# Performance work log

Hardware: AMD Instinct MI355X
Metric: run time of the kernel (lower is better)

## Reference

```python
import jax, jax.numpy as jnp
import numpy as np

N, E, D = 100000, 1600000, 256  # nodes, edges, feature dim
BN_EPS = 1e-5


def _bn(x, g, b):
    # training-mode batchnorm over the node axis (biased variance)
    m = jnp.mean(x, axis=0)
    v = jnp.var(x, axis=0)
    return (x - m) * jax.lax.rsqrt(v + BN_EPS) * g + b


def _gin_layer(h, src, dst, w1, b1, g1, be1, w2, b2, g2=None, be2=None):
    # (1 + eps) * h + sum over in-neighbors; eps = 0
    agg = h + jax.ops.segment_sum(h[src], dst, num_segments=N)
    # MLP(2): Linear -> BN -> ReLU -> Linear
    z = jax.nn.relu(_bn(agg @ w1 + b1, g1, be1))
    z = z @ w2 + b2
    # ApplyNodeFunc wrapper (all but last layer): BN -> ReLU
    if g2 is not None:
        z = jax.nn.relu(_bn(z, g2, be2))
    return z


def setup_inputs() -> dict:
    key = jax.random.key(0)
    ks = jax.random.split(key, 16)
    inp = {}
    inp["x"] = jax.random.normal(ks[0], (N, D), jnp.float32)
    inp["src"] = jax.random.randint(ks[1], (E,), 0, N)
    inp["dst"] = jax.random.randint(ks[2], (E,), 0, N)
    i = 3
    for l in range(3):
        inp[f"l{l}_w1"] = jax.random.normal(ks[i], (D, D), jnp.float32) * 0.02; i += 1
        inp[f"l{l}_b1"] = jnp.zeros((D,), jnp.float32)
        inp[f"l{l}_g1"] = jnp.ones((D,), jnp.float32)
        inp[f"l{l}_be1"] = jnp.zeros((D,), jnp.float32)
        inp[f"l{l}_w2"] = jax.random.normal(ks[i], (D, D), jnp.float32) * 0.02; i += 1
        inp[f"l{l}_b2"] = jnp.zeros((D,), jnp.float32)
        if l < 2:  # last layer: bare MLP, no outer BN/ReLU
            inp[f"l{l}_g2"] = jnp.ones((D,), jnp.float32)
            inp[f"l{l}_be2"] = jnp.zeros((D,), jnp.float32)
    return inp


def reference(x, src, dst,
              l0_w1, l0_b1, l0_g1, l0_be1, l0_w2, l0_b2, l0_g2, l0_be2,
              l1_w1, l1_b1, l1_g1, l1_be1, l1_w2, l1_b2, l1_g2, l1_be2,
              l2_w1, l2_b1, l2_g1, l2_be1, l2_w2, l2_b2):
    # dropout p=0.0 -> identity; residual=False
    h = _gin_layer(x, src, dst, l0_w1, l0_b1, l0_g1, l0_be1, l0_w2, l0_b2, l0_g2, l0_be2)
    h = _gin_layer(h, src, dst, l1_w1, l1_b1, l1_g1, l1_be1, l1_w2, l1_b2, l1_g2, l1_be2)
    h = _gin_layer(h, src, dst, l2_w1, l2_b1, l2_g1, l2_be1, l2_w2, l2_b2)
    return h
```

## Files before the change

kernel.cpp:

```cpp
#include <hip/hip_runtime.h>
#include <hip/hip_bf16.h>
#include <stdint.h>

#define NN 100000
#define DD 256
#define EE 1600000
#define NB 391

typedef short s16x8 __attribute__((ext_vector_type(8)));
typedef float f32x4 __attribute__((ext_vector_type(4)));

__device__ __forceinline__ unsigned short f2bf(float f) {
    union { float f; unsigned int u; } un; un.f = f;
    unsigned int u = un.u;
    unsigned int r = u + 0x7fffu + ((u >> 16) & 1u);
    return (unsigned short)(r >> 16);
}
__device__ __forceinline__ float bf2f(unsigned short s) {
    union { unsigned int u; float f; } c; c.u = (unsigned int)s << 16; return c.f;
}

__global__ void k_wconv(const float* __restrict__ W, unsigned short* __restrict__ Wf) {
    int t = blockIdx.x * 256 + threadIdx.x;
    int j = t & 7;
    int l = (t >> 3) & 63;
    int c = (t >> 9) & 15;
    int s = t >> 13;
    int k   = s * 32 + (l >> 4) * 8 + j;
    int col = c * 16 + (l & 15);
    Wf[t] = f2bf(W[k * 256 + col]);
}

__global__ void k_deghist(const int* __restrict__ dst, int* __restrict__ deg) {
    int e = blockIdx.x * 256 + threadIdx.x;
    atomicAdd(&deg[dst[e]], 1);
}

__global__ void k_blocksum(const int* __restrict__ deg, int* __restrict__ bsum) {
    __shared__ int s[256];
    int t = blockIdx.x * 256 + threadIdx.x;
    s[threadIdx.x] = (t < NN) ? deg[t] : 0;
    __syncthreads();
    for (int off = 128; off > 0; off >>= 1) {
        if (threadIdx.x < off) s[threadIdx.x] += s[threadIdx.x + off];
        __syncthreads();
    }
    if (threadIdx.x == 0) bsum[blockIdx.x] = s[0];
}

__global__ void k_scanb(const int* __restrict__ bsum, int* __restrict__ boff,
                        int* __restrict__ rowptr) {
    __shared__ int s[512];
    int tid = threadIdx.x;
    s[tid] = (tid < NB) ? bsum[tid] : 0;
    __syncthreads();
    for (int off = 1; off < 512; off <<= 1) {
        int x = 0;
        if (tid >= off) x = s[tid - off];
        __syncthreads();
        if (tid >= off) s[tid] += x;
        __syncthreads();
    }
    if (tid < NB) boff[tid] = (tid > 0) ? s[tid - 1] : 0;
    if (tid == 0) rowptr[NN] = EE;
}

__global__ void k_finalscan(const int* __restrict__ deg, const int* __restrict__ boff,
                            int* __restrict__ rowptr) {
    __shared__ int s[256];
    int tid = threadIdx.x;
    int t = blockIdx.x * 256 + tid;
    int v = (t < NN) ? deg[t] : 0;
    s[tid] = v;
    __syncthreads();
    for (int off = 1; off < 256; off <<= 1) {
        int x = 0;
        if (tid >= off) x = s[tid - off];
        __syncthreads();
        if (tid >= off) s[tid] += x;
        __syncthreads();
    }
    if (t < NN) rowptr[t] = boff[blockIdx.x] + s[tid] - v;
}

__global__ void k_fill(const int* __restrict__ src, const int* __restrict__ dst,
                       const int* __restrict__ rowptr, int* __restrict__ cur,
                       int* __restrict__ eidx) {
    int e = blockIdx.x * 256 + threadIdx.x;
    int d = dst[e];
    int pos = atomicAdd(&cur[d], 1);
    eidx[rowptr[d] + pos] = src[e];
}

template<int MODE>
__launch_bounds__(256)
__global__ void k_gather(const void* __restrict__ hv, const int* __restrict__ rowptr,
                         const int* __restrict__ eidx,
                         const float* __restrict__ s1, const float* __restrict__ s2,
                         const float* __restrict__ g, const float* __restrict__ be,
                         ushort4* __restrict__ agg) {
    int gid = blockIdx.x * 256 + threadIdx.x;
    int node = gid >> 6;
    int lane = gid & 63;
    if (node >= NN) return;
    int beg = rowptr[node];
    int end = rowptr[node + 1];
    float4 acc;

    if constexpr (MODE == 0) {
        const float4* h = (const float4*)hv;
        acc = h[(size_t)node * 64 + lane];
        int i = beg;
        for (; i + 8 <= end; i += 8) {
            int idx[8];
            #pragma unroll
            for (int j = 0; j < 8; j++) idx[j] = eidx[i + j];
            float4 v[8];
            #pragma unroll
            for (int j = 0; j < 8; j++) v[j] = h[(size_t)idx[j] * 64 + lane];
            #pragma unroll
            for (int j = 0; j < 8; j++) {
                acc.x += v[j].x; acc.y += v[j].y; acc.z += v[j].z; acc.w += v[j].w;
            }
        }
        for (; i + 4 <= end; i += 4) {
            int idx[4];
            #pragma unroll
            for (int j = 0; j < 4; j++) idx[j] = eidx[i + j];
            float4 v[4];
            #pragma unroll
            for (int j = 0; j < 4; j++) v[j] = h[(size_t)idx[j] * 64 + lane];
            #pragma unroll
            for (int j = 0; j < 4; j++) {
                acc.x += v[j].x; acc.y += v[j].y; acc.z += v[j].z; acc.w += v[j].w;
            }
        }
        for (; i + 2 <= end; i += 2) {
            float4 v0 = h[(size_t)eidx[i] * 64 + lane];
            float4 v1 = h[(size_t)eidx[i + 1] * 64 + lane];
            acc.x += v0.x + v1.x; acc.y += v0.y + v1.y;
            acc.z += v0.z + v1.z; acc.w += v0.w + v1.w;
        }
        if (i < end) {
            float4 v = h[(size_t)eidx[i] * 64 + lane];
            acc.x += v.x; acc.y += v.y; acc.z += v.z; acc.w += v.w;
        }
    } else {
        const ushort4* h = (const ushort4*)hv;
        int c0 = lane * 4;
        float4 s1v = *(const float4*)(s1 + c0);
        float4 s2v = *(const float4*)(s2 + c0);
        float4 gv  = *(const float4*)(g + c0);
        float4 bev = *(const float4*)(be + c0);
        float kk[4], sh[4];
        {
            float m, var;
            m = s1v.x * (1.f/NN); var = s2v.x * (1.f/NN) - m*m; kk[0] = rsqrtf(var+1e-5f)*gv.x; sh[0] = bev.x - m*kk[0];
            m = s1v.y * (1.f/NN); var = s2v.y * (1.f/NN) - m*m; kk[1] = rsqrtf(var+1e-5f)*gv.y; sh[1] = bev.y - m*kk[1];
            m = s1v.z * (1.f/NN); var = s2v.z * (1.f/NN) - m*m; kk[2] = rsqrtf(var+1e-5f)*gv.z; sh[2] = bev.z - m*kk[2];
            m = s1v.w * (1.f/NN); var = s2v.w * (1.f/NN) - m*m; kk[3] = rsqrtf(var+1e-5f)*gv.w; sh[3] = bev.w - m*kk[3];
        }
        ushort4 u = h[(size_t)node * 64 + lane];
        acc.x = fmaxf(bf2f(u.x) * kk[0] + sh[0], 0.f);
        acc.y = fmaxf(bf2f(u.y) * kk[1] + sh[1], 0.f);
        acc.z = fmaxf(bf2f(u.z) * kk[2] + sh[2], 0.f);
        acc.w = fmaxf(bf2f(u.w) * kk[3] + sh[3], 0.f);
        int i = beg;
        for (; i + 8 <= end; i += 8) {
            int idx[8];
            #pragma unroll
            for (int j = 0; j < 8; j++) idx[j] = eidx[i + j];
            ushort4 v[8];
            #pragma unroll
            for (int j = 0; j < 8; j++) v[j] = h[(size_t)idx[j] * 64 + lane];
            #pragma unroll
            for (int j = 0; j < 8; j++) {
                acc.x += fmaxf(bf2f(v[j].x) * kk[0] + sh[0], 0.f);
                acc.y += fmaxf(bf2f(v[j].y) * kk[1] + sh[1], 0.f);
                acc.z += fmaxf(bf2f(v[j].z) * kk[2] + sh[2], 0.f);
                acc.w += fmaxf(bf2f(v[j].w) * kk[3] + sh[3], 0.f);
            }
        }
        for (; i + 4 <= end; i += 4) {
            int idx[4];
            #pragma unroll
            for (int j = 0; j < 4; j++) idx[j] = eidx[i + j];
            ushort4 v[4];
            #pragma unroll
            for (int j = 0; j < 4; j++) v[j] = h[(size_t)idx[j] * 64 + lane];
            #pragma unroll
            for (int j = 0; j < 4; j++) {
                acc.x += fmaxf(bf2f(v[j].x) * kk[0] + sh[0], 0.f);
                acc.y += fmaxf(bf2f(v[j].y) * kk[1] + sh[1], 0.f);
                acc.z += fmaxf(bf2f(v[j].z) * kk[2] + sh[2], 0.f);
                acc.w += fmaxf(bf2f(v[j].w) * kk[3] + sh[3], 0.f);
            }
        }
        for (; i < end; i++) {
            ushort4 a = h[(size_t)eidx[i] * 64 + lane];
            acc.x += fmaxf(bf2f(a.x) * kk[0] + sh[0], 0.f);
            acc.y += fmaxf(bf2f(a.y) * kk[1] + sh[1], 0.f);
            acc.z += fmaxf(bf2f(a.z) * kk[2] + sh[2], 0.f);
            acc.w += fmaxf(bf2f(a.w) * kk[3] + sh[3], 0.f);
        }
    }
    ushort4 o;
    o.x = f2bf(acc.x); o.y = f2bf(acc.y); o.z = f2bf(acc.z); o.w = f2bf(acc.w);
    agg[(size_t)node * 64 + lane] = o;
}

template<bool ABF16, bool BNSTAGE, bool OUTBF16, bool STATS>
__launch_bounds__(256)
__global__ void k_gemm(const void* __restrict__ Av, const unsigned short* __restrict__ Wf,
                       const float* __restrict__ bias,
                       const float* __restrict__ s1, const float* __restrict__ s2,
                       const float* __restrict__ g, const float* __restrict__ be,
                       void* __restrict__ Cv,
                       float* __restrict__ s1o, float* __restrict__ s2o, int M) {
    __shared__ s16x8 Al[2048];
    __shared__ float sbn[512];
    const int tid = threadIdx.x;
    const int base_row = blockIdx.x * 64;

    if constexpr (STATS) {
        sbn[tid] = 0.f; sbn[tid + 256] = 0.f;
    }

    #pragma unroll
    for (int i = 0; i < 8; i++) {
        int chunk = tid + i * 256;
        int row = chunk >> 5;
        int k0  = (chunk & 31) * 8;
        int gr = base_row + row;
        s16x8 sv;
        if constexpr (ABF16) {
            if (gr < M)
                sv = *(const s16x8*)((const unsigned short*)Av + (size_t)gr * 256 + k0);
            else
                sv = (s16x8){0,0,0,0,0,0,0,0};
        } else {
            float vv[8];
            if (gr < M) {
                const float4* gp = (const float4*)((const float*)Av + (size_t)gr * 256 + k0);
                float4 v0 = gp[0], v1 = gp[1];
                vv[0]=v0.x; vv[1]=v0.y; vv[2]=v0.z; vv[3]=v0.w;
                vv[4]=v1.x; vv[5]=v1.y; vv[6]=v1.z; vv[7]=v1.w;
            } else {
                #pragma unroll
                for (int j = 0; j < 8; j++) vv[j] = 0.f;
            }
            if constexpr (BNSTAGE) {
                #pragma unroll
                for (int j = 0; j < 8; j++) {
                    float m  = s1[k0+j] * (1.f/NN);
                    float var = s2[k0+j] * (1.f/NN) - m*m;
                    float kk = rsqrtf(var + 1e-5f) * g[k0+j];
                    float shv = be[k0+j] - m * kk;
                    vv[j] = fmaxf(vv[j] * kk + shv, 0.f);
                }
            }
            #pragma unroll
            for (int j = 0; j < 8; j++) sv[j] = (short)f2bf(vv[j]);
        }
        int byte = (row * 512 + k0 * 2) ^ ((row & 7) << 4);
        Al[byte >> 4] = sv;
    }
    __syncthreads();

    const int lane = tid & 63;
    const int w = tid >> 6;
    const int wr = w >> 1;
    const int wc = w & 1;

    f32x4 acc[2][8];
    #pragma unroll
    for (int m = 0; m < 2; m++)
        #pragma unroll
        for (int c = 0; c < 8; c++)
            acc[m][c] = (f32x4){0.f, 0.f, 0.f, 0.f};

    #pragma unroll
    for (int s = 0; s < 8; s++) {
        s16x8 a[2], b[8];
        #pragma unroll
        for (int m = 0; m < 2; m++) {
            int row = wr * 32 + m * 16 + (lane & 15);
            int koff = s * 32 + (lane >> 4) * 8;
            int byte = (row * 512 + koff * 2) ^ ((row & 7) << 4);
            a[m] = Al[byte >> 4];
        }
        const unsigned short* wp = Wf + (size_t)((s * 16 + wc * 8) * 64 + lane) * 8;
        #pragma unroll
        for (int c = 0; c < 8; c++)
            b[c] = *(const s16x8*)(wp + (size_t)c * 512);
        #pragma unroll
        for (int m = 0; m < 2; m++)
            #pragma unroll
            for (int c = 0; c < 8; c++)
                acc[m][c] = __builtin_amdgcn_mfma_f32_16x16x32_bf16(a[m], b[c], acc[m][c], 0, 0, 0);
    }

    #pragma unroll
    for (int m = 0; m < 2; m++) {
        int row0 = base_row + wr * 32 + m * 16 + (lane >> 4) * 4;
        #pragma unroll
        for (int c = 0; c < 8; c++) {
            int col = wc * 128 + c * 16 + (lane & 15);
            float bv = bias[col];
            float p1 = 0.f, p2 = 0.f;
            #pragma unroll
            for (int r = 0; r < 4; r++) {
                int row = row0 + r;
                if (row < M) {
                    float v = acc[m][c][r] + bv;
                    if constexpr (OUTBF16)
                        ((unsigned short*)Cv)[(size_t)row * 256 + col] = f2bf(v);
                    else
                        ((float*)Cv)[(size_t)row * 256 + col] = v;
                    if constexpr (STATS) { p1 += v; p2 += v * v; }
                }
            }
            if constexpr (STATS) {
                p1 += __shfl_xor(p1, 16); p1 += __shfl_xor(p1, 32);
                p2 += __shfl_xor(p2, 16); p2 += __shfl_xor(p2, 32);
                if (lane < 16) {
                    atomicAdd(&sbn[col], p1);
                    atomicAdd(&sbn[col + 256], p2);
                }
            }
        }
    }
    if constexpr (STATS) {
        __syncthreads();
        atomicAdd(&s1o[tid & 255], sbn[tid]);
        atomicAdd(&s2o[tid & 255], sbn[tid + 256]);
    }
}

extern "C" void kernel_launch(void* const* d_in, const int* in_sizes, int n_in,
                              void* d_out, int out_size, void* d_ws, size_t ws_size,
                              hipStream_t stream) {
    const float* x   = (const float*)d_in[0];
    const int*   src = (const int*)d_in[1];
    const int*   dst = (const int*)d_in[2];
    const float* W[6]    = { (const float*)d_in[3],  (const float*)d_in[7],
                             (const float*)d_in[11], (const float*)d_in[15],
                             (const float*)d_in[19], (const float*)d_in[23] };
    const float* Bias[6] = { (const float*)d_in[4],  (const float*)d_in[8],
                             (const float*)d_in[12], (const float*)d_in[16],
                             (const float*)d_in[20], (const float*)d_in[24] };
    const float* Gam[5]  = { (const float*)d_in[5],  (const float*)d_in[9],
                             (const float*)d_in[13], (const float*)d_in[17],
                             (const float*)d_in[21] };
    const float* Bet[5]  = { (const float*)d_in[6],  (const float*)d_in[10],
                             (const float*)d_in[14], (const float*)d_in[18],
                             (const float*)d_in[22] };

    char* ws = (char*)d_ws;
    unsigned short* Wf = (unsigned short*)ws;
    float* stats = (float*)(ws + 786432);
    unsigned short* aggbf = (unsigned short*)(ws + (1 << 20));
    unsigned short* z2bf  = aggbf + (size_t)NN * DD;
    char* csr = ws + (1 << 20) + 102400000;
    int* rowptr = (int*)csr;
    int* deg    = (int*)(csr + 400128);
    int* cur    = (int*)(csr + 800128);
    int* bsum   = (int*)(csr + 1200128);
    int* boff   = (int*)(csr + 1202176);
    int* eidx   = (int*)(csr + 1204224);
    float* OUT = (float*)d_out;

    for (int i = 0; i < 6; i++)
        k_wconv<<<256, 256, 0, stream>>>(W[i], Wf + (size_t)i * 65536);
    hipMemsetAsync(stats, 0, 5 * 512 * sizeof(float), stream);
    hipMemsetAsync(deg, 0, NN * sizeof(int), stream);
    hipMemsetAsync(cur, 0, NN * sizeof(int), stream);

    k_deghist<<<EE / 256, 256, 0, stream>>>(dst, deg);
    k_blocksum<<<NB, 256, 0, stream>>>(deg, bsum);
    k_scanb<<<1, 512, 0, stream>>>(bsum, boff, rowptr);
    k_finalscan<<<NB, 256, 0, stream>>>(deg, boff, rowptr);
    k_fill<<<EE / 256, 256, 0, stream>>>(src, dst, rowptr, cur, eidx);

    const int GG = (NN * 64 + 255) / 256;
    float* st[5];
    for (int i = 0; i < 5; i++) st[i] = stats + i * 512;

    auto gemm1 = [&](const unsigned short* A, int wi, int si, float* C) {
        k_gemm<true, false, false, true><<<1563, 256, 0, stream>>>(
            A, Wf + (size_t)wi * 65536, Bias[wi], nullptr, nullptr, nullptr, nullptr,
            C, st[si], st[si] + 256, NN);
    };
    auto gemm2bf = [&](const float* A, int wi, int si, int so, unsigned short* C) {
        k_gemm<false, true, true, true><<<1563, 256, 0, stream>>>(
            A, Wf + (size_t)wi * 65536, Bias[wi], st[si], st[si] + 256, Gam[si], Bet[si],
            C, st[so], st[so] + 256, NN);
    };

    k_gather<0><<<GG, 256, 0, stream>>>(x, rowptr, eidx, nullptr, nullptr, nullptr, nullptr,
                                        (ushort4*)aggbf);
    gemm1(aggbf, 0, 0, OUT);
    gemm2bf(OUT, 1, 0, 1, z2bf);

    k_gather<1><<<GG, 256, 0, stream>>>(z2bf, rowptr, eidx, st[1], st[1] + 256, Gam[1], Bet[1],
                                        (ushort4*)aggbf);
    gemm1(aggbf, 2, 2, OUT);
    gemm2bf(OUT, 3, 2, 3, z2bf);

    k_gather<1><<<GG, 256, 0, stream>>>(z2bf, rowptr, eidx, st[3], st[3] + 256, Gam[3], Bet[3],
                                        (ushort4*)aggbf);
    gemm1(aggbf, 4, 4, OUT);
    k_gemm<false, true, false, false><<<1563, 256, 0, stream>>>(
        OUT, Wf + (size_t)5 * 65536, Bias[5], st[4], st[4] + 256, Gam[4], Bet[4],
        OUT, nullptr, nullptr, NN);
}
```

Before: 1.150 ms.

## Feature-slice the gather kernel and convert input features to bf16 first

Gather is restructured so each block handles one of 8 column slices (32 features) for 64 nodes. Within a wave, 4 groups of 16 lanes split the edge list and combine partial sums with shuffles, so each gathered row piece is a 64-byte read. The input x is first converted to bf16 so layer 0 gathers half the bytes. Slicing by features is meant to keep the per-slice working set small enough to hit in L2, and parallelising over edges cuts the serial chain per node. In exchange it adds a conversion pass, extra bf16 rounding of layer-0 inputs, and shorter, less coalesced memory transactions.

```diff
diff --git a/kernel.cpp b/kernel.cpp
--- a/kernel.cpp
+++ b/kernel.cpp
@@ -29,6 +29,15 @@
     int k   = s * 32 + (l >> 4) * 8 + j;
     int col = c * 16 + (l & 15);
     Wf[t] = f2bf(W[k * 256 + col]);
+}
+
+__global__ void k_tobf16(const float4* __restrict__ in, ushort4* __restrict__ out, int n) {
+    for (int i = blockIdx.x * 256 + threadIdx.x; i < n; i += gridDim.x * 256) {
+        float4 v = in[i];
+        ushort4 o;
+        o.x = f2bf(v.x); o.y = f2bf(v.y); o.z = f2bf(v.z); o.w = f2bf(v.w);
+        out[i] = o;
+    }
 }
 
 __global__ void k_deghist(const int* __restrict__ dst, int* __restrict__ deg) {
@@ -94,119 +103,87 @@
 
 template<int MODE>
 __launch_bounds__(256)
-__global__ void k_gather(const void* __restrict__ hv, const int* __restrict__ rowptr,
+__global__ void k_gather(const ushort2* __restrict__ h, const int* __restrict__ rowptr,
                          const int* __restrict__ eidx,
                          const float* __restrict__ s1, const float* __restrict__ s2,
                          const float* __restrict__ g, const float* __restrict__ be,
-                         ushort4* __restrict__ agg) {
-    int gid = blockIdx.x * 256 + threadIdx.x;
-    int node = gid >> 6;
-    int lane = gid & 63;
-    if (node >= NN) return;
-    int beg = rowptr[node];
-    int end = rowptr[node + 1];
-    float4 acc;
-
-    if constexpr (MODE == 0) {
-        const float4* h = (const float4*)hv;
-        acc = h[(size_t)node * 64 + lane];
-        int i = beg;
-        for (; i + 8 <= end; i += 8) {
-            int idx[8];
-            #pragma unroll
-            for (int j = 0; j < 8; j++) idx[j] = eidx[i + j];
-            float4 v[8];
-            #pragma unroll
-            for (int j = 0; j < 8; j++) v[j] = h[(size_t)idx[j] * 64 + lane];
-            #pragma unroll
-            for (int j = 0; j < 8; j++) {
-                acc.x += v[j].x; acc.y += v[j].y; acc.z += v[j].z; acc.w += v[j].w;
-            }
-        }
-        for (; i + 4 <= end; i += 4) {
-            int idx[4];
-            #pragma unroll
-            for (int j = 0; j < 4; j++) idx[j] = eidx[i + j];
-            float4 v[4];
-            #pragma unroll
-            for (int j = 0; j < 4; j++) v[j] = h[(size_t)idx[j] * 64 + lane];
-            #pragma unroll
-            for (int j = 0; j < 4; j++) {
-                acc.x += v[j].x; acc.y += v[j].y; acc.z += v[j].z; acc.w += v[j].w;
-            }
-        }
-        for (; i + 2 <= end; i += 2) {
-            float4 v0 = h[(size_t)eidx[i] * 64 + lane];
-            float4 v1 = h[(size_t)eidx[i + 1] * 64 + lane];
-            acc.x += v0.x + v1.x; acc.y += v0.y + v1.y;
-            acc.z += v0.z + v1.z; acc.w += v0.w + v1.w;
+                         ushort2* __restrict__ agg) {
+    const int slice = blockIdx.x & 7;
+    const int chunk = blockIdx.x >> 3;
+    const int tid  = threadIdx.x;
+    const int wave = tid >> 6;
+    const int lane = tid & 63;
+    const int slot = lane >> 4;
+    const int l16  = lane & 15;
+
+    const ushort2* hp = h + slice * 16 + l16;
+    ushort2* ap = agg + slice * 16 + l16;
+
+    float kk0 = 1.f, kk1 = 1.f, sh0 = 0.f, sh1 = 0.f;
+    if constexpr (MODE == 1) {
+        int c0 = slice * 32 + l16 * 2;
+        float2 s1v = *(const float2*)(s1 + c0);
+        float2 s2v = *(const float2*)(s2 + c0);
+        float2 gv  = *(const float2*)(g + c0);
+        float2 bev = *(const float2*)(be + c0);
+        float m, var;
+        m = s1v.x * (1.f/NN); var = s2v.x * (1.f/NN) - m*m;
+        kk0 = rsqrtf(var + 1e-5f) * gv.x; sh0 = bev.x - m * kk0;
+        m = s1v.y * (1.f/NN); var = s2v.y * (1.f/NN) - m*m;
+        kk1 = rsqrtf(var + 1e-5f) * gv.y; sh1 = bev.y - m * kk1;
+    }
+
+    const int nbase = chunk * 64 + wave * 16;
+    for (int j = 0; j < 16; j++) {
+        int node = nbase + j;
+        if (node >= NN) return;
+        int beg = rowptr[node];
+        int end = rowptr[node + 1];
+
+        float a0 = 0.f, a1 = 0.f, b0 = 0.f, b1 = 0.f;
+        int i = beg + slot;
+        for (; i + 4 < end; i += 8) {
+            int sA = eidx[i];
+            int sB = eidx[i + 4];
+            ushort2 uA = hp[(size_t)sA * 128];
+            ushort2 uB = hp[(size_t)sB * 128];
+            if constexpr (MODE == 1) {
+                a0 += fmaxf(bf2f(uA.x) * kk0 + sh0, 0.f);
+                a1 += fmaxf(bf2f(uA.y) * kk1 + sh1, 0.f);
+                b0 += fmaxf(bf2f(uB.x) * kk0 + sh0, 0.f);
+                b1 += fmaxf(bf2f(uB.y) * kk1 + sh1, 0.f);
+            } else {
+                a0 += bf2f(uA.x); a1 += bf2f(uA.y);
+                b0 += bf2f(uB.x); b1 += bf2f(uB.y);
+            }
         }
         if (i < end) {
-            float4 v = h[(size_t)eidx[i] * 64 + lane];
-            acc.x += v.x; acc.y += v.y; acc.z += v.z; acc.w += v.w;
-        }
-    } else {
-        const ushort4* h = (const ushort4*)hv;
-        int c0 = lane * 4;
-        float4 s1v = *(const float4*)(s1 + c0);
-        float4 s2v = *(const float4*)(s2 + c0);
-        float4 gv  = *(const float4*)(g + c0);
-        float4 bev = *(const float4*)(be + c0);
-        float kk[4], sh[4];
-        {
-            float m, var;
-            m = s1v.x * (1.f/NN); var = s2v.x * (1.f/NN) - m*m; kk[0] = rsqrtf(var+1e-5f)*gv.x; sh[0] = bev.x - m*kk[0];
-            m = s1v.y * (1.f/NN); var = s2v.y * (1.f/NN) - m*m; kk[1] = rsqrtf(var+1e-5f)*gv.y; sh[1] = bev.y - m*kk[1];
-            m = s1v.z * (1.f/NN); var = s2v.z * (1.f/NN) - m*m; kk[2] = rsqrtf(var+1e-5f)*gv.z; sh[2] = bev.z - m*kk[2];
-            m = s1v.w * (1.f/NN); var = s2v.w * (1.f/NN) - m*m; kk[3] = rsqrtf(var+1e-5f)*gv.w; sh[3] = bev.w - m*kk[3];
-        }
-        ushort4 u = h[(size_t)node * 64 + lane];
-        acc.x = fmaxf(bf2f(u.x) * kk[0] + sh[0], 0.f);
-        acc.y = fmaxf(bf2f(u.y) * kk[1] + sh[1], 0.f);
-        acc.z = fmaxf(bf2f(u.z) * kk[2] + sh[2], 0.f);
-        acc.w = fmaxf(bf2f(u.w) * kk[3] + sh[3], 0.f);
-        int i = beg;
-        for (; i + 8 <= end; i += 8) {
-            int idx[8];
-            #pragma unroll
-            for (int j = 0; j < 8; j++) idx[j] = eidx[i + j];
-            ushort4 v[8];
-            #pragma unroll
-            for (int j = 0; j < 8; j++) v[j] = h[(size_t)idx[j] * 64 + lane];
-            #pragma unroll
-            for (int j = 0; j < 8; j++) {
-                acc.x += fmaxf(bf2f(v[j].x) * kk[0] + sh[0], 0.f);
-                acc.y += fmaxf(bf2f(v[j].y) * kk[1] + sh[1], 0.f);
-                acc.z += fmaxf(bf2f(v[j].z) * kk[2] + sh[2], 0.f);
-                acc.w += fmaxf(bf2f(v[j].w) * kk[3] + sh[3], 0.f);
-            }
-        }
-        for (; i + 4 <= end; i += 4) {
-            int idx[4];
-            #pragma unroll
-            for (int j = 0; j < 4; j++) idx[j] = eidx[i + j];
-            ushort4 v[4];
-            #pragma unroll
-            for (int j = 0; j < 4; j++) v[j] = h[(size_t)idx[j] * 64 + lane];
-            #pragma unroll
-            for (int j = 0; j < 4; j++) {
-                acc.x += fmaxf(bf2f(v[j].x) * kk[0] + sh[0], 0.f);
-                acc.y += fmaxf(bf2f(v[j].y) * kk[1] + sh[1], 0.f);
-                acc.z += fmaxf(bf2f(v[j].z) * kk[2] + sh[2], 0.f);
-                acc.w += fmaxf(bf2f(v[j].w) * kk[3] + sh[3], 0.f);
-            }
-        }
-        for (; i < end; i++) {
-            ushort4 a = h[(size_t)eidx[i] * 64 + lane];
-            acc.x += fmaxf(bf2f(a.x) * kk[0] + sh[0], 0.f);
-            acc.y += fmaxf(bf2f(a.y) * kk[1] + sh[1], 0.f);
-            acc.z += fmaxf(bf2f(a.z) * kk[2] + sh[2], 0.f);
-            acc.w += fmaxf(bf2f(a.w) * kk[3] + sh[3], 0.f);
-        }
-    }
-    ushort4 o;
-    o.x = f2bf(acc.x); o.y = f2bf(acc.y); o.z = f2bf(acc.z); o.w = f2bf(acc.w);
-    agg[(size_t)node * 64 + lane] = o;
+            int sA = eidx[i];
+            ushort2 uA = hp[(size_t)sA * 128];
+            if constexpr (MODE == 1) {
+                a0 += fmaxf(bf2f(uA.x) * kk0 + sh0, 0.f);
+                a1 += fmaxf(bf2f(uA.y) * kk1 + sh1, 0.f);
+            } else {
+                a0 += bf2f(uA.x); a1 += bf2f(uA.y);
+            }
+        }
+        a0 += b0; a1 += b1;
+        a0 += __shfl_xor(a0, 16); a0 += __shfl_xor(a0, 32);
+        a1 += __shfl_xor(a1, 16); a1 += __shfl_xor(a1, 32);
+
+        if (slot == 0) {
+            ushort2 u = hp[(size_t)node * 128];
+            if constexpr (MODE == 1) {
+                a0 += fmaxf(bf2f(u.x) * kk0 + sh0, 0.f);
+                a1 += fmaxf(bf2f(u.y) * kk1 + sh1, 0.f);
+            } else {
+                a0 += bf2f(u.x); a1 += bf2f(u.y);
+            }
+            ushort2 o;
+            o.x = f2bf(a0); o.y = f2bf(a1);
+            ap[(size_t)node * 128] = o;
+        }
+    }
 }
 
 template<bool ABF16, bool BNSTAGE, bool OUTBF16, bool STATS>
@@ -382,7 +359,10 @@
     k_finalscan<<<NB, 256, 0, stream>>>(deg, boff, rowptr);
     k_fill<<<EE / 256, 256, 0, stream>>>(src, dst, rowptr, cur, eidx);
 
-    const int GG = (NN * 64 + 255) / 256;
+    k_tobf16<<<8192, 256, 0, stream>>>((const float4*)x, (ushort4*)z2bf, NN * DD / 4);
+
+    const int GCH = (NN + 63) / 64;
+    const int GG  = GCH * 8;
     float* st[5];
     for (int i = 0; i < 5; i++) st[i] = stats + i * 512;
 
@@ -397,18 +377,21 @@
             C, st[so], st[so] + 256, NN);
     };
 
-    k_gather<0><<<GG, 256, 0, stream>>>(x, rowptr, eidx, nullptr, nullptr, nullptr, nullptr,
-                                        (ushort4*)aggbf);
+    k_gather<0><<<GG, 256, 0, stream>>>((const ushort2*)z2bf, rowptr, eidx,
+                                        nullptr, nullptr, nullptr, nullptr,
+                                        (ushort2*)aggbf);
     gemm1(aggbf, 0, 0, OUT);
     gemm2bf(OUT, 1, 0, 1, z2bf);
 
-    k_gather<1><<<GG, 256, 0, stream>>>(z2bf, rowptr, eidx, st[1], st[1] + 256, Gam[1], Bet[1],
-                                        (ushort4*)aggbf);
+    k_gather<1><<<GG, 256, 0, stream>>>((const ushort2*)z2bf, rowptr, eidx,
+                                        st[1], st[1] + 256, Gam[1], Bet[1],
+                                        (ushort2*)aggbf);
     gemm1(aggbf, 2, 2, OUT);
     gemm2bf(OUT, 3, 2, 3, z2bf);
 
-    k_gather<1><<<GG, 256, 0, stream>>>(z2bf, rowptr, eidx, st[3], st[3] + 256, Gam[3], Bet[3],
-                                        (ushort4*)aggbf);
+    k_gather<1><<<GG, 256, 0, stream>>>((const ushort2*)z2bf, rowptr, eidx,
+                                        st[3], st[3] + 256, Gam[3], Bet[3],
+                                        (ushort2*)aggbf);
     gemm1(aggbf, 4, 4, OUT);
     k_gemm<false, true, false, false><<<1563, 256, 0, stream>>>(
         OUT, Wf + (size_t)5 * 65536, Bias[5], st[4], st[4] + 256, Gam[4], Bet[4],
```

Result: slower. 1.617 ms (+40.6%).

## Fuse neighbor gather into first GEMM and store intermediate activations as bf16

Applied to the files above, without the earlier changes.

The separate gather kernel is merged with the first linear layer. Each block aggregates 64 nodes straight into LDS and runs the MFMA GEMM on them, so the bf16 aggregate never goes to global memory. The first GEMM output is now stored as bf16 instead of fp32, halving traffic for the second GEMM's input, and the six weight-conversion launches collapse into one. In exchange, gather latency is serialized per wave over 16 rows before the GEMM, occupancy may drop from the LDS use, and the pre-BN activations lose precision from bf16 rounding.

```diff
diff --git a/kernel.cpp b/kernel.cpp
--- a/kernel.cpp
+++ b/kernel.cpp
@@ -20,15 +20,21 @@
     union { unsigned int u; float f; } c; c.u = (unsigned int)s << 16; return c.f;
 }
 
-__global__ void k_wconv(const float* __restrict__ W, unsigned short* __restrict__ Wf) {
-    int t = blockIdx.x * 256 + threadIdx.x;
+__global__ void k_wconv6(const float* __restrict__ W0, const float* __restrict__ W1,
+                         const float* __restrict__ W2, const float* __restrict__ W3,
+                         const float* __restrict__ W4, const float* __restrict__ W5,
+                         unsigned short* __restrict__ Wf) {
+    int wi = blockIdx.x >> 8;
+    const float* W = wi == 0 ? W0 : wi == 1 ? W1 : wi == 2 ? W2 :
+                     wi == 3 ? W3 : wi == 4 ? W4 : W5;
+    int t = (blockIdx.x & 255) * 256 + threadIdx.x;
     int j = t & 7;
     int l = (t >> 3) & 63;
     int c = (t >> 9) & 15;
     int s = t >> 13;
     int k   = s * 32 + (l >> 4) * 8 + j;
     int col = c * 16 + (l & 15);
-    Wf[t] = f2bf(W[k * 256 + col]);
+    Wf[wi * 65536 + t] = f2bf(W[k * 256 + col]);
 }
 
 __global__ void k_deghist(const int* __restrict__ dst, int* __restrict__ deg) {
@@ -94,124 +100,196 @@
 
 template<int MODE>
 __launch_bounds__(256)
-__global__ void k_gather(const void* __restrict__ hv, const int* __restrict__ rowptr,
+__global__ void k_gathmm(const void* __restrict__ hv, const int* __restrict__ rowptr,
                          const int* __restrict__ eidx,
                          const float* __restrict__ s1, const float* __restrict__ s2,
                          const float* __restrict__ g, const float* __restrict__ be,
-                         ushort4* __restrict__ agg) {
-    int gid = blockIdx.x * 256 + threadIdx.x;
-    int node = gid >> 6;
-    int lane = gid & 63;
-    if (node >= NN) return;
-    int beg = rowptr[node];
-    int end = rowptr[node + 1];
-    float4 acc;
-
-    if constexpr (MODE == 0) {
-        const float4* h = (const float4*)hv;
-        acc = h[(size_t)node * 64 + lane];
-        int i = beg;
-        for (; i + 8 <= end; i += 8) {
-            int idx[8];
-            #pragma unroll
-            for (int j = 0; j < 8; j++) idx[j] = eidx[i + j];
-            float4 v[8];
-            #pragma unroll
-            for (int j = 0; j < 8; j++) v[j] = h[(size_t)idx[j] * 64 + lane];
-            #pragma unroll
-            for (int j = 0; j < 8; j++) {
-                acc.x += v[j].x; acc.y += v[j].y; acc.z += v[j].z; acc.w += v[j].w;
-            }
-        }
-        for (; i + 4 <= end; i += 4) {
-            int idx[4];
-            #pragma unroll
-            for (int j = 0; j < 4; j++) idx[j] = eidx[i + j];
-            float4 v[4];
-            #pragma unroll
-            for (int j = 0; j < 4; j++) v[j] = h[(size_t)idx[j] * 64 + lane];
-            #pragma unroll
-            for (int j = 0; j < 4; j++) {
-                acc.x += v[j].x; acc.y += v[j].y; acc.z += v[j].z; acc.w += v[j].w;
-            }
-        }
-        for (; i + 2 <= end; i += 2) {
-            float4 v0 = h[(size_t)eidx[i] * 64 + lane];
-            float4 v1 = h[(size_t)eidx[i + 1] * 64 + lane];
-            acc.x += v0.x + v1.x; acc.y += v0.y + v1.y;
-            acc.z += v0.z + v1.z; acc.w += v0.w + v1.w;
-        }
-        if (i < end) {
-            float4 v = h[(size_t)eidx[i] * 64 + lane];
-            acc.x += v.x; acc.y += v.y; acc.z += v.z; acc.w += v.w;
-        }
-    } else {
-        const ushort4* h = (const ushort4*)hv;
+                         const unsigned short* __restrict__ Wf,
+                         const float* __restrict__ bias,
+                         unsigned short* __restrict__ C,
+                         float* __restrict__ s1o, float* __restrict__ s2o) {
+    __shared__ s16x8 Al[2048];
+    __shared__ float sbn[512];
+    const int tid = threadIdx.x;
+    const int wave = tid >> 6;
+    const int lane = tid & 63;
+    const int base_row = blockIdx.x * 64;
+
+    sbn[tid] = 0.f; sbn[tid + 256] = 0.f;
+
+    float kk[4], sh[4];
+    if constexpr (MODE == 1) {
         int c0 = lane * 4;
         float4 s1v = *(const float4*)(s1 + c0);
         float4 s2v = *(const float4*)(s2 + c0);
         float4 gv  = *(const float4*)(g + c0);
         float4 bev = *(const float4*)(be + c0);
-        float kk[4], sh[4];
-        {
-            float m, var;
-            m = s1v.x * (1.f/NN); var = s2v.x * (1.f/NN) - m*m; kk[0] = rsqrtf(var+1e-5f)*gv.x; sh[0] = bev.x - m*kk[0];
-            m = s1v.y * (1.f/NN); var = s2v.y * (1.f/NN) - m*m; kk[1] = rsqrtf(var+1e-5f)*gv.y; sh[1] = bev.y - m*kk[1];
-            m = s1v.z * (1.f/NN); var = s2v.z * (1.f/NN) - m*m; kk[2] = rsqrtf(var+1e-5f)*gv.z; sh[2] = bev.z - m*kk[2];
-            m = s1v.w * (1.f/NN); var = s2v.w * (1.f/NN) - m*m; kk[3] = rsqrtf(var+1e-5f)*gv.w; sh[3] = bev.w - m*kk[3];
-        }
-        ushort4 u = h[(size_t)node * 64 + lane];
-        acc.x = fmaxf(bf2f(u.x) * kk[0] + sh[0], 0.f);
-        acc.y = fmaxf(bf2f(u.y) * kk[1] + sh[1], 0.f);
-        acc.z = fmaxf(bf2f(u.z) * kk[2] + sh[2], 0.f);
-        acc.w = fmaxf(bf2f(u.w) * kk[3] + sh[3], 0.f);
-        int i = beg;
-        for (; i + 8 <= end; i += 8) {
-            int idx[8];
+        float m, var;
+        m = s1v.x * (1.f/NN); var = s2v.x * (1.f/NN) - m*m; kk[0] = rsqrtf(var+1e-5f)*gv.x; sh[0] = bev.x - m*kk[0];
+        m = s1v.y * (1.f/NN); var = s2v.y * (1.f/NN) - m*m; kk[1] = rsqrtf(var+1e-5f)*gv.y; sh[1] = bev.y - m*kk[1];
+        m = s1v.z * (1.f/NN); var = s2v.z * (1.f/NN) - m*m; kk[2] = rsqrtf(var+1e-5f)*gv.z; sh[2] = bev.z - m*kk[2];
+        m = s1v.w * (1.f/NN); var = s2v.w * (1.f/NN) - m*m; kk[3] = rsqrtf(var+1e-5f)*gv.w; sh[3] = bev.w - m*kk[3];
+    }
+
+    for (int j = 0; j < 16; j++) {
+        int row = wave * 16 + j;
+        int node = base_row + row;
+        float4 acc = make_float4(0.f, 0.f, 0.f, 0.f);
+        if (node < NN) {
+            int beg = rowptr[node];
+            int end = rowptr[node + 1];
+            if constexpr (MODE == 0) {
+                const float4* h = (const float4*)hv;
+                acc = h[(size_t)node * 64 + lane];
+                int i = beg;
+                for (; i + 8 <= end; i += 8) {
+                    int idx[8];
+                    #pragma unroll
+                    for (int q = 0; q < 8; q++) idx[q] = eidx[i + q];
+                    float4 v[8];
+                    #pragma unroll
+                    for (int q = 0; q < 8; q++) v[q] = h[(size_t)idx[q] * 64 + lane];
+                    #pragma unroll
+                    for (int q = 0; q < 8; q++) {
+                        acc.x += v[q].x; acc.y += v[q].y; acc.z += v[q].z; acc.w += v[q].w;
+                    }
+                }
+                for (; i + 4 <= end; i += 4) {
+                    int idx[4];
+                    #pragma unroll
+                    for (int q = 0; q < 4; q++) idx[q] = eidx[i + q];
+                    float4 v[4];
+                    #pragma unroll
+                    for (int q = 0; q < 4; q++) v[q] = h[(size_t)idx[q] * 64 + lane];
+                    #pragma unroll
+                    for (int q = 0; q < 4; q++) {
+                        acc.x += v[q].x; acc.y += v[q].y; acc.z += v[q].z; acc.w += v[q].w;
+                    }
+                }
+                for (; i < end; i++) {
+                    float4 v = h[(size_t)eidx[i] * 64 + lane];
+                    acc.x += v.x; acc.y += v.y; acc.z += v.z; acc.w += v.w;
+                }
+            } else {
+                const ushort4* h = (const ushort4*)hv;
+                ushort4 u = h[(size_t)node * 64 + lane];
+                acc.x = fmaxf(bf2f(u.x) * kk[0] + sh[0], 0.f);
+                acc.y = fmaxf(bf2f(u.y) * kk[1] + sh[1], 0.f);
+                acc.z = fmaxf(bf2f(u.z) * kk[2] + sh[2], 0.f);
+                acc.w = fmaxf(bf2f(u.w) * kk[3] + sh[3], 0.f);
+                int i = beg;
+                for (; i + 8 <= end; i += 8) {
+                    int idx[8];
+                    #pragma unroll
+                    for (int q = 0; q < 8; q++) idx[q] = eidx[i + q];
+                    ushort4 v[8];
+                    #pragma unroll
+                    for (int q = 0; q < 8; q++) v[q] = h[(size_t)idx[q] * 64 + lane];
+                    #pragma unroll
+                    for (int q = 0; q < 8; q++) {
+                        acc.x += fmaxf(bf2f(v[q].x) * kk[0] + sh[0], 0.f);
+                        acc.y += fmaxf(bf2f(v[q].y) * kk[1] + sh[1], 0.f);
+                        acc.z += fmaxf(bf2f(v[q].z) * kk[2] + sh[2], 0.f);
+                        acc.w += fmaxf(bf2f(v[q].w) * kk[3] + sh[3], 0.f);
+                    }
+                }
+                for (; i + 4 <= end; i += 4) {
+                    int idx[4];
+                    #pragma unroll
+                    for (int q = 0; q < 4; q++) idx[q] = eidx[i + q];
+                    ushort4 v[4];
+                    #pragma unroll
+                    for (int q = 0; q < 4; q++) v[q] = h[(size_t)idx[q] * 64 + lane];
+                    #pragma unroll
+                    for (int q = 0; q < 4; q++) {
+                        acc.x += fmaxf(bf2f(v[q].x) * kk[0] + sh[0], 0.f);
+                        acc.y += fmaxf(bf2f(v[q].y) * kk[1] + sh[1], 0.f);
+                        acc.z += fmaxf(bf2f(v[q].z) * kk[2] + sh[2], 0.f);
+                        acc.w += fmaxf(bf2f(v[q].w) * kk[3] + sh[3], 0.f);
+                    }
+                }
+                for (; i < end; i++) {
+                    ushort4 a = h[(size_t)eidx[i] * 64 + lane];
+                    acc.x += fmaxf(bf2f(a.x) * kk[0] + sh[0], 0.f);
+                    acc.y += fmaxf(bf2f(a.y) * kk[1] + sh[1], 0.f);
+                    acc.z += fmaxf(bf2f(a.z) * kk[2] + sh[2], 0.f);
+                    acc.w += fmaxf(bf2f(a.w) * kk[3] + sh[3], 0.f);
+                }
+            }
+        }
+        ushort4 o;
+        o.x = f2bf(acc.x); o.y = f2bf(acc.y); o.z = f2bf(acc.z); o.w = f2bf(acc.w);
+        int byte = (row * 512 + lane * 8) ^ ((row & 7) << 4);
+        *(ushort4*)((char*)Al + byte) = o;
+    }
+    __syncthreads();
+
+    const int w = wave;
+    const int wr = w >> 1;
+    const int wc = w & 1;
+
+    f32x4 acc[2][8];
+    #pragma unroll
+    for (int m = 0; m < 2; m++)
+        #pragma unroll
+        for (int c = 0; c < 8; c++)
+            acc[m][c] = (f32x4){0.f, 0.f, 0.f, 0.f};
+
+    #pragma unroll
+    for (int s = 0; s < 8; s++) {
+        s16x8 a[2], b[8];
+        #pragma unroll
+        for (int m = 0; m < 2; m++) {
+            int row = wr * 32 + m * 16 + (lane & 15);
+            int koff = s * 32 + (lane >> 4) * 8;
+            int byte = (row * 512 + koff * 2) ^ ((row & 7) << 4);
+            a[m] = Al[byte >> 4];
+        }
+        const unsigned short* wp = Wf + (size_t)((s * 16 + wc * 8) * 64 + lane) * 8;
+        #pragma unroll
+        for (int c = 0; c < 8; c++)
+            b[c] = *(const s16x8*)(wp + (size_t)c * 512);
+        #pragma unroll
+        for (int m = 0; m < 2; m++)
             #pragma unroll
-            for (int j = 0; j < 8; j++) idx[j] = eidx[i + j];
-            ushort4 v[8];
+            for (int c = 0; c < 8; c++)
+                acc[m][c] = __builtin_amdgcn_mfma_f32_16x16x32_bf16(a[m], b[c], acc[m][c], 0, 0, 0);
+    }
+
+    #pragma unroll
+    for (int m = 0; m < 2; m++) {
+        int row0 = base_row + wr * 32 + m * 16 + (lane >> 4) * 4;
+        #pragma unroll
+        for (int c = 0; c < 8; c++) {
+            int col = wc * 128 + c * 16 + (lane & 15);
+            float bv = bias[col];
+            float p1 = 0.f, p2 = 0.f;
             #pragma unroll
-            for (int j = 0; j < 8; j++) v[j] = h[(size_t)idx[j] * 64 + lane];
-            #pragma unroll
-            for (int j = 0; j < 8; j++) {
-                acc.x += fmaxf(bf2f(v[j].x) * kk[0] + sh[0], 0.f);
-                acc.y += fmaxf(bf2f(v[j].y) * kk[1] + sh[1], 0.f);
-                acc.z += fmaxf(bf2f(v[j].z) * kk[2] + sh[2], 0.f);
-                acc.w += fmaxf(bf2f(v[j].w) * kk[3] + sh[3], 0.f);
-            }
-        }
-        for (; i + 4 <= end; i += 4) {
-            int idx[4];
-            #pragma unroll
-            for (int j = 0; j < 4; j++) idx[j] = eidx[i + j];
-            ushort4 v[4];
-            #pragma unroll
-            for (int j = 0; j < 4; j++) v[j] = h[(size_t)idx[j] * 64 + lane];
-            #pragma unroll
-            for (int j = 0; j < 4; j++) {
-                acc.x += fmaxf(bf2f(v[j].x) * kk[0] + sh[0], 0.f);
-                acc.y += fmaxf(bf2f(v[j].y) * kk[1] + sh[1], 0.f);
-                acc.z += fmaxf(bf2f(v[j].z) * kk[2] + sh[2], 0.f);
-                acc.w += fmaxf(bf2f(v[j].w) * kk[3] + sh[3], 0.f);
-            }
-        }
-        for (; i < end; i++) {
-            ushort4 a = h[(size_t)eidx[i] * 64 + lane];
-            acc.x += fmaxf(bf2f(a.x) * kk[0] + sh[0], 0.f);
-            acc.y += fmaxf(bf2f(a.y) * kk[1] + sh[1], 0.f);
-            acc.z += fmaxf(bf2f(a.z) * kk[2] + sh[2], 0.f);
-            acc.w += fmaxf(bf2f(a.w) * kk[3] + sh[3], 0.f);
-        }
-    }
-    ushort4 o;
-    o.x = f2bf(acc.x); o.y = f2bf(acc.y); o.z = f2bf(acc.z); o.w = f2bf(acc.w);
-    agg[(size_t)node * 64 + lane] = o;
-}
-
-template<bool ABF16, bool BNSTAGE, bool OUTBF16, bool STATS>
+            for (int r = 0; r < 4; r++) {
+                int row = row0 + r;
+                if (row < NN) {
+                    float v = acc[m][c][r] + bv;
+                    C[(size_t)row * 256 + col] = f2bf(v);
+                    p1 += v; p2 += v * v;
+                }
+            }
+            p1 += __shfl_xor(p1, 16); p1 += __shfl_xor(p1, 32);
+            p2 += __shfl_xor(p2, 16); p2 += __shfl_xor(p2, 32);
+            if (lane < 16) {
+                atomicAdd(&sbn[col], p1);
+                atomicAdd(&sbn[col + 256], p2);
+            }
+        }
+    }
+    __syncthreads();
+    atomicAdd(&s1o[tid & 255], sbn[tid]);
+    atomicAdd(&s2o[tid & 255], sbn[tid + 256]);
+}
+
+template<bool BNSTAGE, bool OUTBF16, bool STATS>
 __launch_bounds__(256)
-__global__ void k_gemm(const void* __restrict__ Av, const unsigned short* __restrict__ Wf,
+__global__ void k_gemm(const unsigned short* __restrict__ Av,
+                       const unsigned short* __restrict__ Wf,
                        const float* __restrict__ bias,
                        const float* __restrict__ s1, const float* __restrict__ s2,
                        const float* __restrict__ g, const float* __restrict__ be,
@@ -233,34 +311,20 @@
         int k0  = (chunk & 31) * 8;
         int gr = base_row + row;
         s16x8 sv;
-        if constexpr (ABF16) {
-            if (gr < M)
-                sv = *(const s16x8*)((const unsigned short*)Av + (size_t)gr * 256 + k0);
-            else
-                sv = (s16x8){0,0,0,0,0,0,0,0};
-        } else {
-            float vv[8];
-            if (gr < M) {
-                const float4* gp = (const float4*)((const float*)Av + (size_t)gr * 256 + k0);
-                float4 v0 = gp[0], v1 = gp[1];
-                vv[0]=v0.x; vv[1]=v0.y; vv[2]=v0.z; vv[3]=v0.w;
-                vv[4]=v1.x; vv[5]=v1.y; vv[6]=v1.z; vv[7]=v1.w;
-            } else {
-                #pragma unroll
-                for (int j = 0; j < 8; j++) vv[j] = 0.f;
-            }
-            if constexpr (BNSTAGE) {
-                #pragma unroll
-                for (int j = 0; j < 8; j++) {
-                    float m  = s1[k0+j] * (1.f/NN);
-                    float var = s2[k0+j] * (1.f/NN) - m*m;
-                    float kk = rsqrtf(var + 1e-5f) * g[k0+j];
-                    float shv = be[k0+j] - m * kk;
-                    vv[j] = fmaxf(vv[j] * kk + shv, 0.f);
-                }
-            }
+        if (gr < M)
+            sv = *(const s16x8*)(Av + (size_t)gr * 256 + k0);
+        else
+            sv = (s16x8){0,0,0,0,0,0,0,0};
+        if constexpr (BNSTAGE) {
             #pragma unroll
-            for (int j = 0; j < 8; j++) sv[j] = (short)f2bf(vv[j]);
+            for (int j = 0; j < 8; j++) {
+                float m  = s1[k0+j] * (1.f/NN);
+                float var = s2[k0+j] * (1.f/NN) - m*m;
+                float kk = rsqrtf(var + 1e-5f) * g[k0+j];
+                float shv = be[k0+j] - m * kk;
+                float f = fmaxf(bf2f((unsigned short)sv[j]) * kk + shv, 0.f);
+                sv[j] = (short)f2bf(f);
+            }
         }
         int byte = (row * 512 + k0 * 2) ^ ((row & 7) << 4);
         Al[byte >> 4] = sv;
@@ -359,8 +423,8 @@
     char* ws = (char*)d_ws;
     unsigned short* Wf = (unsigned short*)ws;
     float* stats = (float*)(ws + 786432);
-    unsigned short* aggbf = (unsigned short*)(ws + (1 << 20));
-    unsigned short* z2bf  = aggbf + (size_t)NN * DD;
+    unsigned short* z1bf = (unsigned short*)(ws + (1 << 20));
+    unsigned short* z2bf = z1bf + (size_t)NN * DD;
     char* csr = ws + (1 << 20) + 102400000;
     int* rowptr = (int*)csr;
     int* deg    = (int*)(csr + 400128);
@@ -370,8 +434,7 @@
     int* eidx   = (int*)(csr + 1204224);
     float* OUT = (float*)d_out;
 
-    for (int i = 0; i < 6; i++)
-        k_wconv<<<256, 256, 0, stream>>>(W[i], Wf + (size_t)i * 65536);
+    k_wconv6<<<1536, 256, 0, stream>>>(W[0], W[1], W[2], W[3], W[4], W[5], Wf);
     hipMemsetAsync(stats, 0, 5 * 512 * sizeof(float), stream);
     hipMemsetAsync(deg, 0, NN * sizeof(int), stream);
     hipMemsetAsync(cur, 0, NN * sizeof(int), stream);
@@ -382,35 +445,32 @@
     k_finalscan<<<NB, 256, 0, stream>>>(deg, boff, rowptr);
     k_fill<<<EE / 256, 256, 0, stream>>>(src, dst, rowptr, cur, eidx);
 
-    const int GG = (NN * 64 + 255) / 256;
     float* st[5];
     for (int i = 0; i < 5; i++) st[i] = stats + i * 512;
 
-    auto gemm1 = [&](const unsigned short* A, int wi, int si, float* C) {
-        k_gemm<true, false, false, true><<<1563, 256, 0, stream>>>(
-            A, Wf + (size_t)wi * 65536, Bias[wi], nullptr, nullptr, nullptr, nullptr,
-            C, st[si], st[si] + 256, NN);
+    auto gemm2 = [&](const unsigned short* A, int wi, int si, int so, unsigned short* Cb) {
+        k_gemm<true, true, true><<<1563, 256, 0, stream>>>(
+            A, Wf + (size_t)wi * 65536, Bias[wi], st[si], st[si] + 256, Gam[si], Bet[si],
+            Cb, st[so], st[so] + 256, NN);
     };
-    auto gemm2bf = [&](const float* A, int wi, int si, int so, unsigned short* C) {
-        k_gemm<false, true, true, true><<<1563, 256, 0, stream>>>(
-            A, Wf + (size_t)wi * 65536, Bias[wi], st[si], st[si] + 256, Gam[si], Bet[si],
-            C, st[so], st[so] + 256, NN);
-    };
-
-    k_gather<0><<<GG, 256, 0, stream>>>(x, rowptr, eidx, nullptr, nullptr, nullptr, nullptr,
-                                        (ushort4*)aggbf);
-    gemm1(aggbf, 0, 0, OUT);
-    gemm2bf(OUT, 1, 0, 1, z2bf);
-
-    k_gather<1><<<GG, 256, 0, stream>>>(z2bf, rowptr, eidx, st[1], st[1] + 256, Gam[1], Bet[1],
-                                        (ushort4*)aggbf);
-    gemm1(aggbf, 2, 2, OUT);
-    gemm2bf(OUT, 3, 2, 3, z2bf);
-
-    k_gather<1><<<GG, 256, 0, stream>>>(z2bf, rowptr, eidx, st[3], st[3] + 256, Gam[3], Bet[3],
-                                        (ushort4*)aggbf);
-    gemm1(aggbf, 4, 4, OUT);
-    k_gemm<false, true, false, false><<<1563, 256, 0, stream>>>(
-        OUT, Wf + (size_t)5 * 65536, Bias[5], st[4], st[4] + 256, Gam[4], Bet[4],
+
+    k_gathmm<0><<<1563, 256, 0, stream>>>(x, rowptr, eidx,
+                                          nullptr, nullptr, nullptr, nullptr,
+                                          Wf + (size_t)0 * 65536, Bias[0],
+                                          z1bf, st[0], st[0] + 256);
+    gemm2(z1bf, 1, 0, 1, z2bf);
+
+    k_gathmm<1><<<1563, 256, 0, stream>>>(z2bf, rowptr, eidx,
+                                          st[1], st[1] + 256, Gam[1], Bet[1],
+                                          Wf + (size_t)2 * 65536, Bias[2],
+                                          z1bf, st[2], st[2] + 256);
+    gemm2(z1bf, 3, 2, 3, z2bf);
+
+    k_gathmm<1><<<1563, 256, 0, stream>>>(z2bf, rowptr, eidx,
+                                          st[3], st[3] + 256, Gam[3], Bet[3],
+                                          Wf + (size_t)4 * 65536, Bias[4],
+                                          z1bf, st[4], st[4] + 256);
+    k_gemm<true, false, false><<<1563, 256, 0, stream>>>(
+        z1bf, Wf + (size_t)5 * 65536, Bias[5], st[4], st[4] + 256, Gam[4], Bet[4],
         OUT, nullptr, nullptr, NN);
 }
```

After: 1.153 ms. About the same (+0.2%).
